# Kernel optimization log

Measured on AMD Instinct MI355X. Metric: run time of the kernel, lower is better.

Reference implementation:

```python
import jax, jax.numpy as jnp
import numpy as np

N = 50000      # nodes
E = 1600000    # edges (avg degree 32)
NF = 128       # hidden_nf
L = 4          # n_layers
EA = 1         # edge_attr_nf


def setup_inputs() -> dict:
    key = jax.random.key(0)
    ks = jax.random.split(key, 10)
    return {
        "pos": jax.random.normal(ks[0], (N, 3), jnp.float32),
        "v": jax.random.normal(ks[1], (N, 3), jnp.float32),
        "edge_attr": jax.random.normal(ks[2], (E, EA), jnp.float32),
        # phi: Linear(1+EA -> NF), SiLU, Linear(NF -> 1, no bias), Tanh
        "phi_w1": jax.random.normal(ks[3], (L, 1 + EA, NF), jnp.float32) * 0.1,
        "phi_b1": jnp.zeros((L, NF), jnp.float32),
        "phi_w2": jax.random.normal(ks[4], (L, NF, 1), jnp.float32) * 0.001,
        # coord_mlp_vel: Linear(1 -> NF), SiLU, Linear(NF -> 1)
        "vel_w1": jax.random.normal(ks[5], (L, 1, NF), jnp.float32) * 0.1,
        "vel_b1": jnp.zeros((L, NF), jnp.float32),
        "vel_w2": jax.random.normal(ks[6], (L, NF, 1), jnp.float32) * 0.1,
        "vel_b2": jnp.zeros((L, 1), jnp.float32),
        "edge_index": jax.random.randint(ks[7], (2, E), 0, N, dtype=jnp.int64),
    }


def _layer(x, vel_norm, v, row, col, edge_attr,
           pw1, pb1, pw2, vw1, vb1, vw2, vb2):
    # edge model: gather endpoints, radial feature, per-edge MLP
    x_diff = x[row] - x[col]                                        # [E,3]
    radial = jnp.sqrt(jnp.sum(x_diff * x_diff, axis=1, keepdims=True))  # [E,1]
    e_in = jnp.concatenate([radial, edge_attr], axis=1)             # [E,1+EA]
    h = jax.nn.silu(e_in @ pw1 + pb1)                               # [E,NF]
    e_out = jnp.tanh(h @ pw2)                                       # [E,1]
    m = x_diff * e_out                                              # [E,3]
    # node model: segment mean over receiving node (row)
    agg = jax.ops.segment_sum(m, row, num_segments=N)               # [N,3]
    cnt = jax.ops.segment_sum(jnp.ones((row.shape[0], 1), x.dtype), row,
                              num_segments=N)                        # [N,1]
    x = x + agg / jnp.maximum(cnt, 1.0)
    # velocity term: x += v * coord_mlp_vel(||v||)
    phi_v = jax.nn.silu(vel_norm @ vw1 + vb1) @ vw2 + vb2           # [N,1]
    return x + v * phi_v


def reference(pos, v, edge_attr, phi_w1, phi_b1, phi_w2,
              vel_w1, vel_b1, vel_w2, vel_b2, edge_index):
    row, col = edge_index[0], edge_index[1]
    vel_norm = jnp.sqrt(jnp.sum(v * v, axis=1, keepdims=True))      # [N,1]
    x = pos
    for i in range(L):
        x = _layer(x, vel_norm, v, row, col, edge_attr,
                   phi_w1[i], phi_b1[i], phi_w2[i],
                   vel_w1[i], vel_b1[i], vel_w2[i], vel_b2[i])
    return x
```

## Files before the change

### kernel.cpp

```cpp
#include <hip/hip_runtime.h>
#include <hip/hip_fp16.h>

#define NF 128
#define NL 4

#define NR 384
#define RMAXF 48.0f
#define NA 128
#define AMINF -8.0f
#define ARANGE 16.0f
#define AQMAX 511
#define NV 512
#define VMAXF 8.0f

#define BROWS_SHIFT 7
#define BROWS 128
#define NBMAX 512
#define BCAP 4480
#define EPT 16
#define EPB 4096

struct __align__(8) Half4 { __half2 lo; __half2 hi; };

__device__ __forceinline__ float fast_sigmoid(float x) {
    float z = __builtin_amdgcn_exp2f(-1.44269504f * x);
    return __builtin_amdgcn_rcpf(1.0f + z);
}
__device__ __forceinline__ float silu(float x) { return x * fast_sigmoid(x); }

__device__ __forceinline__ float fast_tanh(float x) {
    float y = fminf(fmaxf(x, -15.0f), 15.0f);
    float e2 = __builtin_amdgcn_exp2f(2.88539008f * y);
    return (e2 - 1.0f) * __builtin_amdgcn_rcpf(e2 + 1.0f);
}

__global__ __launch_bounds__(256) void setup1_kernel(
    const float* __restrict__ pw1, const float* __restrict__ pb1,
    const float* __restrict__ pw2, const float* __restrict__ vw1,
    const float* __restrict__ vb1, const float* __restrict__ vw2,
    const float* __restrict__ vb2,
    __half* __restrict__ etabh, float* __restrict__ vtab,
    int* __restrict__ counts, int* __restrict__ cursor)
{
    int t = blockIdx.x * 256 + threadIdx.x;
    if (t < NBMAX) counts[t] = 0;
    if (t == 0) *cursor = 0;

    if (t < NL * NR * NA) {
        int l = t / (NR * NA), rem = t - l * NR * NA;
        int ri = rem / NA, ai = rem - ri * NA;
        float r = ri * (RMAXF / (NR - 1));
        float a = AMINF + ai * (ARANGE / (NA - 1));
        const float* w1r = pw1 + l * 2 * NF;
        const float* w1a = w1r + NF;
        const float* b1  = pb1 + l * NF;
        const float* w2  = pw2 + l * NF;
        float acc = 0.f;
        #pragma unroll 8
        for (int k = 0; k < NF; ++k) {
            float pre = fmaf(r, w1r[k], fmaf(a, w1a[k], b1[k]));
            acc = fmaf(silu(pre), w2[k], acc);
        }
        etabh[t] = __float2half(fast_tanh(acc));
    } else if (t < NL * NR * NA + NL * NV) {
        int u = t - NL * NR * NA;
        int l = u / NV, vi = u - l * NV;
        float vn = vi * (VMAXF / (NV - 1));
        const float* w1 = vw1 + l * NF;
        const float* b1 = vb1 + l * NF;
        const float* w2 = vw2 + l * NF;
        float acc = 0.f;
        #pragma unroll 8
        for (int k = 0; k < NF; ++k) {
            float pre = fmaf(vn, w1[k], b1[k]);
            acc = fmaf(silu(pre), w2[k], acc);
        }
        vtab[u] = acc + vb2[l];
    }
}

__global__ __launch_bounds__(256) void setup2_kernel(
    const __half* __restrict__ etabh, Half4* __restrict__ tab,
    const float* __restrict__ pos, const float* __restrict__ v,
    const float* __restrict__ vtab,
    float4* __restrict__ x4A, float4* __restrict__ v4,
    float* __restrict__ phv, int N)
{
    int t = blockIdx.x * 256 + threadIdx.x;
    if (t < NL * NR * NA) {
        int rem = t % (NR * NA);
        int ri = rem / NA, ai = rem - ri * NA;
        int da = (ai + 1 < NA) ? 1  : 0;
        int dr = (ri + 1 < NR) ? NA : 0;
        __half h00 = etabh[t];
        __half h01 = etabh[t + da];
        __half h10 = etabh[t + dr];
        __half h11 = etabh[t + dr + da];
        Half4 h;
        h.lo = __halves2half2(h00, h01);
        h.hi = __halves2half2(h10, h11);
        tab[t] = h;
    }
    if (t < N) {
        x4A[t] = make_float4(pos[t*3], pos[t*3+1], pos[t*3+2], 0.f);
        float vx = v[t*3], vy = v[t*3+1], vz = v[t*3+2];
        v4[t] = make_float4(vx, vy, vz, 0.f);
        float vn = sqrtf(vx*vx + vy*vy + vz*vz);
        float vt = fminf(vn * ((NV - 1) / VMAXF), NV - 1.0002f);
        int k0 = (int)vt; float fv = vt - (float)k0;
        #pragma unroll
        for (int l = 0; l < NL; ++l) {
            const float* vt_l = vtab + l * NV;
            phv[l * N + t] = fmaf(fv, vt_l[k0+1] - vt_l[k0], vt_l[k0]);
        }
    }
}

__global__ __launch_bounds__(256) void passA_kernel(
    const int* __restrict__ row, const int* __restrict__ col,
    const float* __restrict__ ea, int* __restrict__ counts,
    unsigned int* __restrict__ coarse, int E)
{
    __shared__ int hist[NBMAX];
    __shared__ int base[NBMAX];
    int tid = threadIdx.x;
    for (int i = tid; i < NBMAX; i += 256) hist[i] = 0;
    __syncthreads();
    int e0 = blockIdx.x * EPB;
    unsigned int rec[EPT];
    int bin[EPT];
    int rank[EPT];
    #pragma unroll
    for (int k = 0; k < EPT; ++k) {
        int e = e0 + k * 256 + tid;
        bin[k] = -1;
        if (e < E) {
            int r = row[e];
            int c = col[e];
            float a = fminf(fmaxf(ea[e], AMINF), AMINF + ARANGE);
            int aq = (int)fmaf(a - AMINF, (float)AQMAX / ARANGE, 0.5f);
            bin[k]  = r >> BROWS_SHIFT;
            rec[k]  = ((unsigned int)(r & (BROWS - 1)) << 25) |
                      ((unsigned int)c << 9) | (unsigned int)aq;
            rank[k] = atomicAdd(&hist[bin[k]], 1);
        }
    }
    __syncthreads();
    for (int i = tid; i < NBMAX; i += 256) {
        int h = hist[i];
        base[i] = (h > 0) ? atomicAdd(&counts[i], h) : 0;
    }
    __syncthreads();
    #pragma unroll
    for (int k = 0; k < EPT; ++k) {
        if (bin[k] >= 0) {
            int p = base[bin[k]] + rank[k];
            if (p < BCAP) coarse[(size_t)bin[k] * BCAP + p] = rec[k];
        }
    }
}

__global__ __launch_bounds__(256) void passB_kernel(
    const unsigned int* __restrict__ coarse, const int* __restrict__ counts,
    int* __restrict__ cursor, unsigned int* __restrict__ slots,
    int2* __restrict__ sc, int N)
{
    __shared__ unsigned int recs[BCAP];
    __shared__ int hist[BROWS];
    __shared__ int excl[BROWS];
    __shared__ int cur[BROWS];
    __shared__ int cb_sh;
    int b = blockIdx.x, tid = threadIdx.x;
    int n = min(counts[b], BCAP);
    if (tid == 0) cb_sh = atomicAdd(cursor, n);
    for (int i = tid; i < n; i += 256) recs[i] = coarse[(size_t)b * BCAP + i];
    if (tid < BROWS) hist[tid] = 0;
    __syncthreads();
    for (int i = tid; i < n; i += 256) atomicAdd(&hist[recs[i] >> 25], 1);
    __syncthreads();
    if (tid < BROWS) excl[tid] = hist[tid];
    __syncthreads();
    for (int d = 1; d < BROWS; d <<= 1) {
        int vv = 0;
        if (tid < BROWS && tid >= d) vv = excl[tid - d];
        __syncthreads();
        if (tid < BROWS) excl[tid] += vv;
        __syncthreads();
    }
    int cb = cb_sh;
    if (tid < BROWS) {
        int e = excl[tid] - hist[tid];
        excl[tid] = e;
        cur[tid]  = e;
        int r = b * BROWS + tid;
        if (r < N) sc[r] = make_int2(cb + e, hist[tid]);
    }
    __syncthreads();
    for (int i = tid; i < n; i += 256) {
        unsigned int rc = recs[i];
        int p = atomicAdd(&cur[rc >> 25], 1);
        slots[cb + p] = rc & 0x01FFFFFFu;
    }
}

__global__ __launch_bounds__(256) void layer_kernel(
    const float4* __restrict__ xo, float4* __restrict__ xn4,
    float* __restrict__ xn3,
    const unsigned int* __restrict__ slots, const int2* __restrict__ sc,
    const Half4* __restrict__ tab, const float4* __restrict__ v4,
    const float* __restrict__ phv, int n)
{
    int sub = threadIdx.x & 15;
    int r = blockIdx.x * 16 + (threadIdx.x >> 4);
    if (r >= n) return;
    int2 s = sc[r];
    float4 xr = xo[r];
    float mx = 0.f, my = 0.f, mz = 0.f;
    for (int j = sub; j < s.y; j += 16) {
        unsigned int rec = slots[s.x + j];
        int c = (int)(rec >> 9);
        float at = (float)(rec & 511u) * ((NA - 1) / (float)AQMAX);
        float4 xc = xo[c];
        float dx = xr.x - xc.x, dy = xr.y - xc.y, dz = xr.z - xc.z;
        float rad = sqrtf(dx*dx + dy*dy + dz*dz);
        float rt = fminf(rad * ((NR - 1) / RMAXF), NR - 1.0002f);
        int i0 = (int)rt; float fr = rt - (float)i0;
        int j0 = (int)at; float fa = at - (float)j0;
        Half4 p = tab[i0 * NA + j0];
        float v00 = __low2float(p.lo),  v01 = __high2float(p.lo);
        float v10 = __low2float(p.hi),  v11 = __high2float(p.hi);
        float top = fmaf(fa, v01 - v00, v00);
        float bot = fmaf(fa, v11 - v10, v10);
        float e   = fmaf(fr, bot - top, top);
        mx = fmaf(dx, e, mx); my = fmaf(dy, e, my); mz = fmaf(dz, e, mz);
    }
    #pragma unroll
    for (int d = 1; d < 16; d <<= 1) {
        mx += __shfl_xor(mx, d);
        my += __shfl_xor(my, d);
        mz += __shfl_xor(mz, d);
    }
    if (sub == 0) {
        float inv = __builtin_amdgcn_rcpf(fmaxf((float)s.y, 1.0f));
        float4 vv = v4[r];
        float ph = phv[r];
        float ox = fmaf(mx, inv, fmaf(vv.x, ph, xr.x));
        float oy = fmaf(my, inv, fmaf(vv.y, ph, xr.y));
        float oz = fmaf(mz, inv, fmaf(vv.z, ph, xr.z));
        if (xn3) { xn3[r*3+0] = ox; xn3[r*3+1] = oy; xn3[r*3+2] = oz; }
        else     { xn4[r] = make_float4(ox, oy, oz, 0.f); }
    }
}

extern "C" void kernel_launch(void* const* d_in, const int* in_sizes, int n_in,
                              void* d_out, int out_size, void* d_ws, size_t ws_size,
                              hipStream_t stream) {
    const float* pos = (const float*)d_in[0];
    const float* v   = (const float*)d_in[1];
    const float* ea  = (const float*)d_in[2];
    const float* pw1 = (const float*)d_in[3];
    const float* pb1 = (const float*)d_in[4];
    const float* pw2 = (const float*)d_in[5];
    const float* vw1 = (const float*)d_in[6];
    const float* vb1 = (const float*)d_in[7];
    const float* vw2 = (const float*)d_in[8];
    const float* vb2 = (const float*)d_in[9];
    const int*   ei  = (const int*)d_in[10];

    const int N = in_sizes[0] / 3;
    const int E = in_sizes[10] / 2;
    const int* row = ei;
    const int* col = ei + E;
    const int nb = (N + BROWS - 1) >> BROWS_SHIFT;

    char*   ws  = (char*)d_ws;
    float4* x4A = (float4*)ws;
    float4* x4B = x4A + N;
    float4* v4  = x4B + N;
    Half4*  tab = (Half4*)(v4 + N);
    unsigned int* coarse = (unsigned int*)(tab + (size_t)NL * NR * NA);
    unsigned int* slots  = coarse + (size_t)nb * BCAP;
    int2*   sc     = (int2*)(slots + E);
    float*  phv    = (float*)(sc + N);
    __half* etabh  = (__half*)(phv + (size_t)NL * N);
    float*  vtab   = (float*)(etabh + (size_t)NL * NR * NA);
    int*    counts = (int*)(vtab + (size_t)NL * NV);
    int*    cursor = counts + NBMAX;

    float* x = (float*)d_out;
    dim3 blk(256);

    int t1 = NL * NR * NA + NL * NV;
    setup1_kernel<<<(t1 + 255)/256, blk, 0, stream>>>(
        pw1, pb1, pw2, vw1, vb1, vw2, vb2, etabh, vtab, counts, cursor);
    int t2 = NL * NR * NA;
    setup2_kernel<<<(t2 + 255)/256, blk, 0, stream>>>(
        etabh, tab, pos, v, vtab, x4A, v4, phv, N);
    passA_kernel<<<(E + EPB - 1)/EPB, blk, 0, stream>>>(row, col, ea, counts, coarse, E);
    passB_kernel<<<nb, blk, 0, stream>>>(coarse, counts, cursor, slots, sc, N);

    int gR = (N + 15) / 16;
    const size_t TSZ = (size_t)NR * NA;
    layer_kernel<<<gR, blk, 0, stream>>>(x4A, x4B, nullptr, slots, sc, tab + 0*TSZ, v4, phv + 0*(size_t)N, N);
    layer_kernel<<<gR, blk, 0, stream>>>(x4B, x4A, nullptr, slots, sc, tab + 1*TSZ, v4, phv + 1*(size_t)N, N);
    layer_kernel<<<gR, blk, 0, stream>>>(x4A, x4B, nullptr, slots, sc, tab + 2*TSZ, v4, phv + 2*(size_t)N, N);
    layer_kernel<<<gR, blk, 0, stream>>>(x4B, nullptr, x,   slots, sc, tab + 3*TSZ, v4, phv + 3*(size_t)N, N);
}
```

Baseline: 120.3 us.

## Drop per-row sort pass; aggregate coarse row-bins with LDS atomics

Removes the second binning pass (passB) that sorted edges into exact per-row CSR slots. Edges are now only bucketed into bins of 32 rows, and each layer kernel processes one bin per block, summing messages and counts into shared memory with atomics. passA is also restructured into a count pass followed by a scatter pass over 8192 edges per block. This saves a kernel launch and a full scatter/read of the edge array, at the cost of LDS float atomic contention in every layer. It also brings nondeterministic summation order, and silently drops edges if a bin exceeds the fixed capacity of 1344.

Result: slower. 198.8 us (+65.2%).

```diff
diff --git a/kernel.cpp b/kernel.cpp
--- a/kernel.cpp
+++ b/kernel.cpp
@@ -13,12 +13,11 @@
 #define NV 512
 #define VMAXF 8.0f
 
-#define BROWS_SHIFT 7
-#define BROWS 128
-#define NBMAX 512
-#define BCAP 4480
-#define EPT 16
-#define EPB 4096
+#define B2SHIFT 5
+#define B2ROWS 32
+#define NBMAX 2048
+#define BCAP 1344
+#define EPB 8192
 
 struct __align__(8) Half4 { __half2 lo; __half2 hi; };
 
@@ -40,11 +39,10 @@
     const float* __restrict__ vb1, const float* __restrict__ vw2,
     const float* __restrict__ vb2,
     __half* __restrict__ etabh, float* __restrict__ vtab,
-    int* __restrict__ counts, int* __restrict__ cursor)
+    int* __restrict__ counts)
 {
     int t = blockIdx.x * 256 + threadIdx.x;
     if (t < NBMAX) counts[t] = 0;
-    if (t == 0) *cursor = 0;
 
     if (t < NL * NR * NA) {
         int l = t / (NR * NA), rem = t - l * NR * NA;
@@ -92,13 +90,9 @@
         int ri = rem / NA, ai = rem - ri * NA;
         int da = (ai + 1 < NA) ? 1  : 0;
         int dr = (ri + 1 < NR) ? NA : 0;
-        __half h00 = etabh[t];
-        __half h01 = etabh[t + da];
-        __half h10 = etabh[t + dr];
-        __half h11 = etabh[t + dr + da];
         Half4 h;
-        h.lo = __halves2half2(h00, h01);
-        h.hi = __halves2half2(h10, h11);
+        h.lo = __halves2half2(etabh[t], etabh[t + da]);
+        h.hi = __halves2half2(etabh[t + dr], etabh[t + dr + da]);
         tab[t] = h;
     }
     if (t < N) {
@@ -122,133 +116,103 @@
     unsigned int* __restrict__ coarse, int E)
 {
     __shared__ int hist[NBMAX];
-    __shared__ int base[NBMAX];
     int tid = threadIdx.x;
     for (int i = tid; i < NBMAX; i += 256) hist[i] = 0;
     __syncthreads();
     int e0 = blockIdx.x * EPB;
-    unsigned int rec[EPT];
-    int bin[EPT];
-    int rank[EPT];
-    #pragma unroll
-    for (int k = 0; k < EPT; ++k) {
-        int e = e0 + k * 256 + tid;
-        bin[k] = -1;
-        if (e < E) {
-            int r = row[e];
-            int c = col[e];
-            float a = fminf(fmaxf(ea[e], AMINF), AMINF + ARANGE);
-            int aq = (int)fmaf(a - AMINF, (float)AQMAX / ARANGE, 0.5f);
-            bin[k]  = r >> BROWS_SHIFT;
-            rec[k]  = ((unsigned int)(r & (BROWS - 1)) << 25) |
-                      ((unsigned int)c << 9) | (unsigned int)aq;
-            rank[k] = atomicAdd(&hist[bin[k]], 1);
-        }
-    }
+    int e1 = min(e0 + EPB, E);
+    for (int e = e0 + tid; e < e1; e += 256)
+        atomicAdd(&hist[row[e] >> B2SHIFT], 1);
     __syncthreads();
     for (int i = tid; i < NBMAX; i += 256) {
         int h = hist[i];
-        base[i] = (h > 0) ? atomicAdd(&counts[i], h) : 0;
-    }
-    __syncthreads();
-    #pragma unroll
-    for (int k = 0; k < EPT; ++k) {
-        if (bin[k] >= 0) {
-            int p = base[bin[k]] + rank[k];
-            if (p < BCAP) coarse[(size_t)bin[k] * BCAP + p] = rec[k];
-        }
-    }
-}
-
-__global__ __launch_bounds__(256) void passB_kernel(
-    const unsigned int* __restrict__ coarse, const int* __restrict__ counts,
-    int* __restrict__ cursor, unsigned int* __restrict__ slots,
-    int2* __restrict__ sc, int N)
-{
-    __shared__ unsigned int recs[BCAP];
-    __shared__ int hist[BROWS];
-    __shared__ int excl[BROWS];
-    __shared__ int cur[BROWS];
-    __shared__ int cb_sh;
-    int b = blockIdx.x, tid = threadIdx.x;
-    int n = min(counts[b], BCAP);
-    if (tid == 0) cb_sh = atomicAdd(cursor, n);
-    for (int i = tid; i < n; i += 256) recs[i] = coarse[(size_t)b * BCAP + i];
-    if (tid < BROWS) hist[tid] = 0;
-    __syncthreads();
-    for (int i = tid; i < n; i += 256) atomicAdd(&hist[recs[i] >> 25], 1);
-    __syncthreads();
-    if (tid < BROWS) excl[tid] = hist[tid];
-    __syncthreads();
-    for (int d = 1; d < BROWS; d <<= 1) {
-        int vv = 0;
-        if (tid < BROWS && tid >= d) vv = excl[tid - d];
-        __syncthreads();
-        if (tid < BROWS) excl[tid] += vv;
-        __syncthreads();
-    }
-    int cb = cb_sh;
-    if (tid < BROWS) {
-        int e = excl[tid] - hist[tid];
-        excl[tid] = e;
-        cur[tid]  = e;
-        int r = b * BROWS + tid;
-        if (r < N) sc[r] = make_int2(cb + e, hist[tid]);
-    }
-    __syncthreads();
-    for (int i = tid; i < n; i += 256) {
-        unsigned int rc = recs[i];
-        int p = atomicAdd(&cur[rc >> 25], 1);
-        slots[cb + p] = rc & 0x01FFFFFFu;
+        int base = (h > 0) ? atomicAdd(&counts[i], h) : 0;
+        hist[i] = base;
+    }
+    __syncthreads();
+    for (int e = e0 + tid; e < e1; e += 256) {
+        int r = row[e];
+        int c = col[e];
+        float a = fminf(fmaxf(ea[e], AMINF), AMINF + ARANGE);
+        int aq = (int)fmaf(a - AMINF, (float)AQMAX / ARANGE, 0.5f);
+        int bin = r >> B2SHIFT;
+        unsigned int rec = ((unsigned int)(r & (B2ROWS - 1)) << 26) |
+                           ((unsigned int)c << 9) | (unsigned int)aq;
+        int p = atomicAdd(&hist[bin], 1);
+        if (p < BCAP) coarse[(size_t)bin * BCAP + p] = rec;
     }
 }
 
 __global__ __launch_bounds__(256) void layer_kernel(
     const float4* __restrict__ xo, float4* __restrict__ xn4,
     float* __restrict__ xn3,
-    const unsigned int* __restrict__ slots, const int2* __restrict__ sc,
+    const unsigned int* __restrict__ coarse, const int* __restrict__ counts,
     const Half4* __restrict__ tab, const float4* __restrict__ v4,
-    const float* __restrict__ phv, int n)
-{
-    int sub = threadIdx.x & 15;
-    int r = blockIdx.x * 16 + (threadIdx.x >> 4);
-    if (r >= n) return;
-    int2 s = sc[r];
-    float4 xr = xo[r];
-    float mx = 0.f, my = 0.f, mz = 0.f;
-    for (int j = sub; j < s.y; j += 16) {
-        unsigned int rec = slots[s.x + j];
-        int c = (int)(rec >> 9);
-        float at = (float)(rec & 511u) * ((NA - 1) / (float)AQMAX);
-        float4 xc = xo[c];
-        float dx = xr.x - xc.x, dy = xr.y - xc.y, dz = xr.z - xc.z;
-        float rad = sqrtf(dx*dx + dy*dy + dz*dz);
-        float rt = fminf(rad * ((NR - 1) / RMAXF), NR - 1.0002f);
-        int i0 = (int)rt; float fr = rt - (float)i0;
-        int j0 = (int)at; float fa = at - (float)j0;
-        Half4 p = tab[i0 * NA + j0];
-        float v00 = __low2float(p.lo),  v01 = __high2float(p.lo);
-        float v10 = __low2float(p.hi),  v11 = __high2float(p.hi);
-        float top = fmaf(fa, v01 - v00, v00);
-        float bot = fmaf(fa, v11 - v10, v10);
-        float e   = fmaf(fr, bot - top, top);
-        mx = fmaf(dx, e, mx); my = fmaf(dy, e, my); mz = fmaf(dz, e, mz);
-    }
-    #pragma unroll
-    for (int d = 1; d < 16; d <<= 1) {
-        mx += __shfl_xor(mx, d);
-        my += __shfl_xor(my, d);
-        mz += __shfl_xor(mz, d);
-    }
-    if (sub == 0) {
-        float inv = __builtin_amdgcn_rcpf(fmaxf((float)s.y, 1.0f));
-        float4 vv = v4[r];
-        float ph = phv[r];
-        float ox = fmaf(mx, inv, fmaf(vv.x, ph, xr.x));
-        float oy = fmaf(my, inv, fmaf(vv.y, ph, xr.y));
-        float oz = fmaf(mz, inv, fmaf(vv.z, ph, xr.z));
-        if (xn3) { xn3[r*3+0] = ox; xn3[r*3+1] = oy; xn3[r*3+2] = oz; }
-        else     { xn4[r] = make_float4(ox, oy, oz, 0.f); }
+    const float* __restrict__ phv, int N)
+{
+    __shared__ float4 xr_s[B2ROWS];
+    __shared__ float aggx[B2ROWS], aggy[B2ROWS], aggz[B2ROWS];
+    __shared__ int cnti[B2ROWS];
+    int b = blockIdx.x, tid = threadIdx.x;
+    int r0 = b << B2SHIFT;
+    int n = min(counts[b], BCAP);
+    if (tid < B2ROWS) {
+        int r = r0 + tid;
+        xr_s[tid] = (r < N) ? xo[r] : make_float4(0.f, 0.f, 0.f, 0.f);
+        aggx[tid] = 0.f; aggy[tid] = 0.f; aggz[tid] = 0.f; cnti[tid] = 0;
+    }
+    __syncthreads();
+    const unsigned int* my = coarse + (size_t)b * BCAP;
+
+    #define PROCESS(REC) do {                                               \
+        unsigned int rec_ = (REC);                                          \
+        int rl_ = rec_ >> 26;                                               \
+        int c_  = (rec_ >> 9) & 0x1FFFF;                                    \
+        float at_ = (float)(rec_ & 511u) * ((NA - 1) / (float)AQMAX);       \
+        float4 xc_ = xo[c_];                                                \
+        float4 xr_ = xr_s[rl_];                                             \
+        float dx_ = xr_.x - xc_.x, dy_ = xr_.y - xc_.y, dz_ = xr_.z - xc_.z;\
+        float rad_ = sqrtf(dx_*dx_ + dy_*dy_ + dz_*dz_);                    \
+        float rt_ = fminf(rad_ * ((NR - 1) / RMAXF), NR - 1.0002f);         \
+        int i0_ = (int)rt_; float fr_ = rt_ - (float)i0_;                   \
+        int j0_ = (int)at_; float fa_ = at_ - (float)j0_;                   \
+        Half4 p_ = tab[i0_ * NA + j0_];                                     \
+        float v00_ = __low2float(p_.lo),  v01_ = __high2float(p_.lo);       \
+        float v10_ = __low2float(p_.hi),  v11_ = __high2float(p_.hi);       \
+        float top_ = fmaf(fa_, v01_ - v00_, v00_);                          \
+        float bot_ = fmaf(fa_, v11_ - v10_, v10_);                          \
+        float e_   = fmaf(fr_, bot_ - top_, top_);                          \
+        atomicAdd(&aggx[rl_], dx_ * e_);                                    \
+        atomicAdd(&aggy[rl_], dy_ * e_);                                    \
+        atomicAdd(&aggz[rl_], dz_ * e_);                                    \
+        atomicAdd(&cnti[rl_], 1);                                           \
+    } while (0)
+
+    int i = tid;
+    for (; i + 256 < n; i += 512) {
+        unsigned int rec0 = my[i];
+        unsigned int rec1 = my[i + 256];
+        PROCESS(rec0);
+        PROCESS(rec1);
+    }
+    if (i < n) PROCESS(my[i]);
+    #undef PROCESS
+
+    __syncthreads();
+    if (tid < B2ROWS) {
+        int r = r0 + tid;
+        if (r < N) {
+            int m = cnti[tid];
+            float inv = __builtin_amdgcn_rcpf(fmaxf((float)m, 1.0f));
+            float4 xr = xr_s[tid];
+            float4 vv = v4[r];
+            float ph = phv[r];
+            float ox = fmaf(aggx[tid], inv, fmaf(vv.x, ph, xr.x));
+            float oy = fmaf(aggy[tid], inv, fmaf(vv.y, ph, xr.y));
+            float oz = fmaf(aggz[tid], inv, fmaf(vv.z, ph, xr.z));
+            if (xn3) { xn3[r*3+0] = ox; xn3[r*3+1] = oy; xn3[r*3+2] = oz; }
+            else     { xn4[r] = make_float4(ox, oy, oz, 0.f); }
+        }
     }
 }
 
@@ -271,7 +235,7 @@
     const int E = in_sizes[10] / 2;
     const int* row = ei;
     const int* col = ei + E;
-    const int nb = (N + BROWS - 1) >> BROWS_SHIFT;
+    const int nb = (N + B2ROWS - 1) >> B2SHIFT;
 
     char*   ws  = (char*)d_ws;
     float4* x4A = (float4*)ws;
@@ -279,30 +243,25 @@
     float4* v4  = x4B + N;
     Half4*  tab = (Half4*)(v4 + N);
     unsigned int* coarse = (unsigned int*)(tab + (size_t)NL * NR * NA);
-    unsigned int* slots  = coarse + (size_t)nb * BCAP;
-    int2*   sc     = (int2*)(slots + E);
-    float*  phv    = (float*)(sc + N);
+    float*  phv    = (float*)(coarse + (size_t)nb * BCAP);
     __half* etabh  = (__half*)(phv + (size_t)NL * N);
     float*  vtab   = (float*)(etabh + (size_t)NL * NR * NA);
     int*    counts = (int*)(vtab + (size_t)NL * NV);
-    int*    cursor = counts + NBMAX;
 
     float* x = (float*)d_out;
     dim3 blk(256);
 
     int t1 = NL * NR * NA + NL * NV;
     setup1_kernel<<<(t1 + 255)/256, blk, 0, stream>>>(
-        pw1, pb1, pw2, vw1, vb1, vw2, vb2, etabh, vtab, counts, cursor);
+        pw1, pb1, pw2, vw1, vb1, vw2, vb2, etabh, vtab, counts);
     int t2 = NL * NR * NA;
     setup2_kernel<<<(t2 + 255)/256, blk, 0, stream>>>(
         etabh, tab, pos, v, vtab, x4A, v4, phv, N);
     passA_kernel<<<(E + EPB - 1)/EPB, blk, 0, stream>>>(row, col, ea, counts, coarse, E);
-    passB_kernel<<<nb, blk, 0, stream>>>(coarse, counts, cursor, slots, sc, N);
-
-    int gR = (N + 15) / 16;
+
     const size_t TSZ = (size_t)NR * NA;
-    layer_kernel<<<gR, blk, 0, stream>>>(x4A, x4B, nullptr, slots, sc, tab + 0*TSZ, v4, phv + 0*(size_t)N, N);
-    layer_kernel<<<gR, blk, 0, stream>>>(x4B, x4A, nullptr, slots, sc, tab + 1*TSZ, v4, phv + 1*(size_t)N, N);
-    layer_kernel<<<gR, blk, 0, stream>>>(x4A, x4B, nullptr, slots, sc, tab + 2*TSZ, v4, phv + 2*(size_t)N, N);
-    layer_kernel<<<gR, blk, 0, stream>>>(x4B, nullptr, x,   slots, sc, tab + 3*TSZ, v4, phv + 3*(size_t)N, N);
-}
+    layer_kernel<<<nb, blk, 0, stream>>>(x4A, x4B, nullptr, coarse, counts, tab + 0*TSZ, v4, phv + 0*(size_t)N, N);
+    layer_kernel<<<nb, blk, 0, stream>>>(x4B, x4A, nullptr, coarse, counts, tab + 1*TSZ, v4, phv + 1*(size_t)N, N);
+    layer_kernel<<<nb, blk, 0, stream>>>(x4A, x4B, nullptr, coarse, counts, tab + 2*TSZ, v4, phv + 2*(size_t)N, N);
+    layer_kernel<<<nb, blk, 0, stream>>>(x4B, nullptr, x,   coarse, counts, tab + 3*TSZ, v4, phv + 3*(size_t)N, N);
+}
```
